# Kernel tuning notes

Hardware: AMD Instinct MI355X
Metric: run time of the kernel (lower is better)

## Reference

```python
import jax, jax.numpy as jnp
import numpy as np
from jax import lax

B, C_IN = 8192, 1

def _conv(x, w, b):
    # x: [N,C,H,W], w: [O,I,kh,kw] valid conv, stride 1
    y = lax.conv_general_dilated(x, w, window_strides=(1, 1), padding='VALID',
                                 dimension_numbers=('NCHW', 'OIHW', 'NCHW'))
    return y + b[None, :, None, None]

def _maxpool2(x):
    return lax.reduce_window(x, -jnp.inf, lax.max, (1, 1, 2, 2), (1, 1, 2, 2), 'VALID')

def setup_inputs() -> dict:
    key = jax.random.key(0)
    ks = jax.random.split(key, 9)
    def kaiming(k, shape, fan_in):
        return jax.random.normal(k, shape, jnp.float32) * np.float32(1.0 / np.sqrt(fan_in))
    x = jax.random.normal(ks[0], (B, C_IN, 28, 28), jnp.float32)
    w1 = kaiming(ks[1], (10, C_IN, 5, 5), C_IN * 25)
    b1 = kaiming(ks[2], (10,), C_IN * 25)
    w2 = kaiming(ks[3], (20, 10, 5, 5), 10 * 25)
    b2 = kaiming(ks[4], (20,), 10 * 25)
    wl1 = kaiming(ks[5], (50, 320), 320)
    bl1 = kaiming(ks[6], (50,), 320)
    wl2 = kaiming(ks[7], (10, 50), 50)
    bl2 = kaiming(ks[8], (10,), 50)
    return {"x": x, "w1": w1, "b1": b1, "w2": w2, "b2": b2,
            "wl1": wl1, "bl1": bl1, "wl2": wl2, "bl2": bl2}

def reference(x, w1, b1, w2, b2, wl1, bl1, wl2, bl2):
    h = jax.nn.relu(_conv(x, w1, b1))       # [B,10,24,24]
    h = _maxpool2(h)                         # [B,10,12,12]
    h = jax.nn.relu(_conv(h, w2, b2))        # [B,20,8,8]
    h = _maxpool2(h)                         # [B,20,4,4]
    h = h.reshape(h.shape[0], -1)            # [B,320]
    h = jax.nn.relu(h @ wl1.T + bl1)         # [B,50]
    return h @ wl2.T + bl2                   # [B,10]
```

## Files before the change

### kernel.cpp

```cpp
#include <hip/hip_runtime.h>

#define THREADS 256
#define IPB 4

typedef _Float16 f16;
typedef _Float16 f16x2 __attribute__((ext_vector_type(2)));
typedef _Float16 f16x4 __attribute__((ext_vector_type(4)));
typedef _Float16 f16x8 __attribute__((ext_vector_type(8)));
typedef float f32x2 __attribute__((ext_vector_type(2)));
typedef float f32x4 __attribute__((ext_vector_type(4)));
typedef float f32x16 __attribute__((ext_vector_type(16)));
typedef unsigned int uint;

__device__ __forceinline__ f16x2 pkrtz(float a, float b) {
    return __builtin_bit_cast(f16x2, __builtin_amdgcn_cvt_pkrtz(a, b));
}
template<int CTRL>
__device__ __forceinline__ float dppmax(float v) {
    const int i = __builtin_bit_cast(int, v);
    const int s = __builtin_amdgcn_update_dpp(i, i, CTRL, 0xF, 0xF, true);
    return fmaxf(v, __builtin_bit_cast(float, s));
}
__device__ __forceinline__ f16x8 ldpairs(const unsigned char* a) {
    const uint* p = (const uint*)a;
    uint4 u;
    u.x = p[0]; u.y = p[2]; u.z = p[4]; u.w = p[6];
    return __builtin_bit_cast(f16x8, u);
}

#define P1C 24
#define P1R 288
#define P1I 3456
#define XH  13824
#define SMEM_BYTES 20224

__global__ void pack_weights(const float* __restrict__ w1,
                             const float* __restrict__ w2,
                             const float* __restrict__ wl1,
                             unsigned char* __restrict__ ws) {
    f16x8* w2af = (f16x8*)(ws + 1024);
    f16x8* wl1pk = (f16x8*)(ws + 17408);
    const int gid = blockIdx.x * blockDim.x + threadIdx.x;
    const int gsz = gridDim.x * blockDim.x;
    for (int e = gid; e < 1000; e += gsz) {
        const int s = e / 40, r = e - s * 40;
        const int oc = r >> 1, h = r & 1;
        f16x8 a;
        #pragma unroll
        for (int j = 0; j < 8; ++j) {
            const int ic = h * 8 + j;
            a[j] = (f16)(ic < 10 ? w2[(oc * 10 + ic) * 25 + s] : 0.f);
        }
        w2af[e] = a;
    }
    for (int e = gid; e < 2560; e += gsz) {
        const int tile = e / 640, rem = e % 640;
        const int s = rem / 64, lane = rem % 64;
        const int m = lane & 15, quad = lane >> 4;
        const int hh = tile * 16 + m;
        f16x8 a;
        #pragma unroll
        for (int j = 0; j < 8; ++j)
            a[j] = (f16)(hh < 50 ? wl1[hh * 320 + s * 32 + quad * 8 + j] : 0.f);
        wl1pk[e] = a;
    }
}

__global__ __launch_bounds__(THREADS, 8)
void lenet_one(const float* __restrict__ x,
               const unsigned char* __restrict__ ws,
               const float* __restrict__ w1, const float* __restrict__ b1,
               const float* __restrict__ b2,
               const float* __restrict__ bl1,
               const float* __restrict__ wl2, const float* __restrict__ bl2,
               float* __restrict__ out, int batch)
{
    __shared__ __align__(16) unsigned char smem[SMEM_BYTES];
    f16*   p2h = (f16*)smem;
    float* h1  = (float*)(smem + 2624);

    const f16x8* w2af  = (const f16x8*)(ws + 1024);
    const f16x8* wl1pk = (const f16x8*)(ws + 17408);

    const int tid = threadIdx.x;
    const int lane = tid & 63;
    const int wv_ = tid >> 6;
    const int n15 = lane & 15;
    const int q4  = lane >> 4;
    const int cM = lane & 31, hK = lane >> 5;

    f16x8 A1 = {}, A2 = {};
    if (n15 < 10) {
        #pragma unroll
        for (int j = 0; j < 5; ++j) A1[j] = (f16)w1[n15 * 25 + q4 * 5 + j];
        if (q4 == 0) {
            #pragma unroll
            for (int j = 0; j < 5; ++j) A2[j] = (f16)w1[n15 * 25 + 20 + j];
        }
        if (q4 == 1) A2[0] = (f16)b1[n15];
    }

    #pragma unroll 1
    for (int sub = 0; sub < 2; ++sub) {
        if (tid < 112) {
            const int rr = tid >> 2, imL = (tid >> 1) & 1, half = tid & 1;
            const int ig = min(blockIdx.x * IPB + sub * 2 + imL, batch - 1);
            const float* xp = x + (size_t)ig * 784 + rr * 28 + half * 14;
            float v[15];
            #pragma unroll
            for (int t = 0; t < 7; ++t) {
                const f32x2 a = *(const f32x2*)(xp + 2 * t);
                v[2 * t] = a[0]; v[2 * t + 1] = a[1];
            }
            v[14] = half ? 0.f : xp[14];
            uint* pw = (uint*)(smem + XH + rr * 224 + imL * 112) + half * 14;
            #pragma unroll
            for (int t = 0; t < 7; ++t) {
                uint2 w;
                w.x = __builtin_bit_cast(uint, pkrtz(v[2 * t], v[2 * t + 1]));
                w.y = __builtin_bit_cast(uint, pkrtz(v[2 * t + 1], v[2 * t + 2]));
                *(uint2*)(pw + 2 * t) = w;
            }
        } else if (tid >= 224) {
            *(uint*)(smem + XH + 28 * 224 + (tid - 224) * 4) = 0;
        }
        __syncthreads();

        {
            const int imL = wv_ >> 1, oxg = wv_ & 1;
            const int ox = oxg * 16 + n15;
            const int im = sub * 2 + imL;
            const unsigned char* pb = smem + XH + imL * 112 + ox * 4
                                    + q4 * 224;
            unsigned char* wbase = smem + im * P1I;
            f16x8 hA0 = {}, hB0 = {}, hA1 = {}, hB1 = {};
            #pragma unroll
            for (int uu = 0; uu < 12; ++uu) {
                const int u = 11 - uu;
                const f16x8 B1a = ldpairs(pb + (2 * u) * 224);
                const f16x8 B1b = ldpairs(pb + (2 * u + 1) * 224);
                f16x8 B2a, B2b;
                if (u >= 10) {
                    B2a = ldpairs(pb - q4 * 224 + (2 * u + 4) * 224);
                    B2b = ldpairs(pb - q4 * 224 + (2 * u + 5) * 224);
                } else {
                    B2a = (u & 1) ? hA1 : hA0;
                    B2b = (u & 1) ? hB1 : hB0;
                }
                if (u & 1) { hA1 = B1a; hB1 = B1b; }
                else       { hA0 = B1a; hB0 = B1b; }
                if (q4 == 1) { B2a[0] = (f16)1.f; B2b[0] = (f16)1.f; }
                f32x4 aa = {0.f, 0.f, 0.f, 0.f}, ab = {0.f, 0.f, 0.f, 0.f};
                aa = __builtin_amdgcn_mfma_f32_16x16x32_f16(A1, B1a, aa, 0, 0, 0);
                ab = __builtin_amdgcn_mfma_f32_16x16x32_f16(A1, B1b, ab, 0, 0, 0);
                aa = __builtin_amdgcn_mfma_f32_16x16x32_f16(A2, B2a, aa, 0, 0, 0);
                ab = __builtin_amdgcn_mfma_f32_16x16x32_f16(A2, B2b, ab, 0, 0, 0);
                float vr[4];
                #pragma unroll
                for (int r = 0; r < 4; ++r) {
                    float v = fmaxf(aa[r], ab[r]);
                    v = dppmax<0xB1>(v);
                    vr[r] = fmaxf(v, 0.f);
                }
                if (!(lane & 1) && q4 < 3 && (oxg == 0 || n15 < 8)) {
                    const int px = oxg * 8 + (n15 >> 1);
                    f16x2 o0, o1;
                    o0[0] = (f16)vr[0]; o0[1] = (f16)vr[1];
                    o1[0] = (f16)vr[2]; o1[1] = (f16)vr[3];
                    uint2 w;
                    w.x = __builtin_bit_cast(uint, o0);
                    w.y = __builtin_bit_cast(uint, o1);
                    *(uint2*)(wbase + u * P1R + px * P1C + q4 * 8) = w;
                }
            }
        }
        __syncthreads();
    }

    {
        const int cy = cM >> 3, cx = cM & 7;
        const int afoff = (cM < 20 ? cM : 19) * 2 + hK;
        int bb[2];
        #pragma unroll
        for (int q = 0; q < 2; ++q) {
            const int t = wv_ * 2 + q, im = t >> 1, h2 = t & 1;
            bb[q] = im * P1I + (4 * h2 + cy) * P1R + cx * P1C + hK * 16;
        }
        f32x16 acc[2];
        #pragma unroll
        for (int q = 0; q < 2; ++q)
            #pragma unroll
            for (int r = 0; r < 16; ++r) acc[q][r] = 0.f;
        #pragma unroll 1
        for (int ky = 0; ky < 5; ++ky) {
            #pragma unroll
            for (int kx = 0; kx < 5; ++kx) {
                const f16x8 a = w2af[(ky * 5 + kx) * 40 + afoff];
                #pragma unroll
                for (int q = 0; q < 2; ++q) {
                    const unsigned char* ad = smem + bb[q] + ky * P1R + kx * P1C;
                    const f16x4 lo = *(const f16x4*)(ad);
                    const f16x4 hi = *(const f16x4*)(ad + 8);
                    f16x8 b;
                    #pragma unroll
                    for (int j = 0; j < 4; ++j) { b[j] = lo[j]; b[4 + j] = hi[j]; }
                    acc[q] = __builtin_amdgcn_mfma_f32_32x32x16_f16(a, b, acc[q],
                                                                    0, 0, 0);
                }
            }
        }
        __syncthreads();
        #pragma unroll
        for (int q = 0; q < 2; ++q) {
            const int t = wv_ * 2 + q, im = t >> 1, h2 = t & 1;
            #pragma unroll
            for (int r = 0; r < 16; ++r) {
                const int m = (r & 3) + 8 * (r >> 2) + 4 * hK;
                float v = acc[q][r];
                v = dppmax<0xB1>(v);
                v = dppmax<0x128>(v);
                if (m < 20 && (lane & 9) == 0) {
                    const int py = 2 * h2 + (cM >> 4), px = cx >> 1;
                    p2h[im * 328 + m * 16 + py * 4 + px] =
                        (f16)fmaxf(v + b2[m], 0.f);
                }
            }
        }
    }
    __syncthreads();

    {
        f32x4 facc = {0.f, 0.f, 0.f, 0.f};
        #pragma unroll 1
        for (int s = 0; s < 10; ++s) {
            const f16x8 a = wl1pk[(wv_ * 10 + s) * 64 + lane];
            f16x8 b = {};
            if (n15 < IPB)
                b = *(const f16x8*)(p2h + n15 * 328 + s * 32 + q4 * 8);
            facc = __builtin_amdgcn_mfma_f32_16x16x32_f16(a, b, facc, 0, 0, 0);
        }
        if (n15 < IPB) {
            #pragma unroll
            for (int r = 0; r < 4; ++r) {
                const int h = wv_ * 16 + q4 * 4 + r;
                if (h < 50)
                    h1[n15 * 52 + h] = fmaxf(facc[r] + bl1[h], 0.f);
            }
        }
    }
    __syncthreads();

    if (tid < IPB * 10) {
        const int im = tid / 10, o = tid % 10;
        const int imgo = min(blockIdx.x * IPB + im, batch - 1);
        float a = bl2[o];
        #pragma unroll
        for (int h = 0; h < 50; ++h)
            a += h1[im * 52 + h] * wl2[o * 50 + h];
        out[(size_t)imgo * 10 + o] = a;
    }
}

extern "C" void kernel_launch(void* const* d_in, const int* in_sizes, int n_in,
                              void* d_out, int out_size, void* d_ws, size_t ws_size,
                              hipStream_t stream) {
    const float* x   = (const float*)d_in[0];
    const float* w1  = (const float*)d_in[1];
    const float* b1  = (const float*)d_in[2];
    const float* w2  = (const float*)d_in[3];
    const float* b2  = (const float*)d_in[4];
    const float* wl1 = (const float*)d_in[5];
    const float* bl1 = (const float*)d_in[6];
    const float* wl2 = (const float*)d_in[7];
    const float* bl2 = (const float*)d_in[8];
    float* out = (float*)d_out;
    unsigned char* ws = (unsigned char*)d_ws;

    const int batch = in_sizes[0] / 784;
    pack_weights<<<64, 256, 0, stream>>>(w1, w2, wl1, ws);
    const int grid = (batch + IPB - 1) / IPB;
    lenet_one<<<grid, THREADS, 0, stream>>>(x, ws, w1, b1, b2, bl1, wl2, bl2,
                                            out, batch);
}
```

Baseline: 119.6 us.

## Swizzle pool1 shared layout and store pool2 outputs channel-contiguous

XOR-swizzles the column offset of the pool1 activation tile in shared memory by row, for both the writes and the conv2 MFMA operand reads, to reduce LDS bank conflicts. The pool2 output is changed to a position-major, channel-contiguous layout so each lane writes four f16 values in one vector store instead of scalar stores. The fc1 weight packing is permuted to match the new flattening order. This touches three stages that must agree on layout, so any mismatch would corrupt results.

After: 121.3 us. Within noise of the previous version (+1.4%).

```diff
diff --git a/kernel.cpp b/kernel.cpp
--- a/kernel.cpp
+++ b/kernel.cpp
@@ -33,6 +33,7 @@
 #define P1I 3456
 #define XH  13824
 #define SMEM_BYTES 20224
+
 
 __global__ void pack_weights(const float* __restrict__ w1,
                              const float* __restrict__ w2,
@@ -56,12 +57,15 @@
     for (int e = gid; e < 2560; e += gsz) {
         const int tile = e / 640, rem = e % 640;
         const int s = rem / 64, lane = rem % 64;
-        const int m = lane & 15, quad = lane >> 4;
-        const int hh = tile * 16 + m;
+        const int m16 = lane & 15, quad = lane >> 4;
+        const int hh = tile * 16 + m16;
         f16x8 a;
         #pragma unroll
-        for (int j = 0; j < 8; ++j)
-            a[j] = (f16)(hh < 50 ? wl1[hh * 320 + s * 32 + quad * 8 + j] : 0.f);
+        for (int j = 0; j < 8; ++j) {
+            const int kp = s * 32 + quad * 8 + j;
+            const int pos = kp / 20, mm = kp - pos * 20;
+            a[j] = (f16)(hh < 50 ? wl1[hh * 320 + mm * 16 + pos] : 0.f);
+        }
         wl1pk[e] = a;
     }
 }
@@ -170,7 +174,8 @@
                     uint2 w;
                     w.x = __builtin_bit_cast(uint, o0);
                     w.y = __builtin_bit_cast(uint, o1);
-                    *(uint2*)(wbase + u * P1R + px * P1C + q4 * 8) = w;
+                    const int Cw = (px * P1C + q4 * 8) ^ ((u & 3) << 3);
+                    *(uint2*)(wbase + u * P1R + Cw) = w;
                 }
             }
         }
@@ -180,12 +185,13 @@
     {
         const int cy = cM >> 3, cx = cM & 7;
         const int afoff = (cM < 20 ? cM : 19) * 2 + hK;
-        int bb[2];
+        int rowb[2];
         #pragma unroll
         for (int q = 0; q < 2; ++q) {
             const int t = wv_ * 2 + q, im = t >> 1, h2 = t & 1;
-            bb[q] = im * P1I + (4 * h2 + cy) * P1R + cx * P1C + hK * 16;
-        }
+            rowb[q] = im * P1I + (4 * h2 + cy) * P1R;
+        }
+        const int Cb = cx * P1C + hK * 16;
         f32x16 acc[2];
         #pragma unroll
         for (int q = 0; q < 2; ++q)
@@ -193,14 +199,17 @@
             for (int r = 0; r < 16; ++r) acc[q][r] = 0.f;
         #pragma unroll 1
         for (int ky = 0; ky < 5; ++ky) {
+            const int Kk = ((cy + ky) & 3) << 3;
             #pragma unroll
             for (int kx = 0; kx < 5; ++kx) {
                 const f16x8 a = w2af[(ky * 5 + kx) * 40 + afoff];
+                const int Clo = (Cb + kx * P1C) ^ Kk;
+                const int Chi = (Cb + kx * P1C + 8) ^ Kk;
                 #pragma unroll
                 for (int q = 0; q < 2; ++q) {
-                    const unsigned char* ad = smem + bb[q] + ky * P1R + kx * P1C;
-                    const f16x4 lo = *(const f16x4*)(ad);
-                    const f16x4 hi = *(const f16x4*)(ad + 8);
+                    const unsigned char* rp = smem + rowb[q] + ky * P1R;
+                    const f16x4 lo = *(const f16x4*)(rp + Clo);
+                    const f16x4 hi = *(const f16x4*)(rp + Chi);
                     f16x8 b;
                     #pragma unroll
                     for (int j = 0; j < 4; ++j) { b[j] = lo[j]; b[4 + j] = hi[j]; }
@@ -213,17 +222,22 @@
         #pragma unroll
         for (int q = 0; q < 2; ++q) {
             const int t = wv_ * 2 + q, im = t >> 1, h2 = t & 1;
-            #pragma unroll
-            for (int r = 0; r < 16; ++r) {
-                const int m = (r & 3) + 8 * (r >> 2) + 4 * hK;
-                float v = acc[q][r];
-                v = dppmax<0xB1>(v);
-                v = dppmax<0x128>(v);
-                if (m < 20 && (lane & 9) == 0) {
-                    const int py = 2 * h2 + (cM >> 4), px = cx >> 1;
-                    p2h[im * 328 + m * 16 + py * 4 + px] =
-                        (f16)fmaxf(v + b2[m], 0.f);
-                }
+            const int py = 2 * h2 + (cM >> 4), px = (cM & 7) >> 1;
+            f16* base = p2h + im * 328 + (py * 4 + px) * 20 + 4 * hK;
+            #pragma unroll
+            for (int g = 0; g < 4; ++g) {
+                const int m0 = 8 * g + 4 * hK;
+                f16x4 vv;
+                #pragma unroll
+                for (int e = 0; e < 4; ++e) {
+                    const int r = 4 * g + e;
+                    float v = acc[q][r];
+                    v = dppmax<0xB1>(v);
+                    v = dppmax<0x128>(v);
+                    vv[e] = (f16)fmaxf(v + b2[min(m0 + e, 19)], 0.f);
+                }
+                if ((lane & 9) == 0 && m0 < 20)
+                    *(f16x4*)(base + 8 * g) = vv;
             }
         }
     }
```
